# Kernel tuning notes

Measured on AMD Instinct MI355X. Metric: run time of the kernel, lower is better.

Reference implementation:

```python
import jax, jax.numpy as jnp
import numpy as np

K = 2        # kernel_size
DIL = 1      # dilation
H = 768      # h_size = nhid + nout
NOUT = 256
NLAYER = 10  # weight-tied iterations of f_theta


def conv1d(x, w, b, dilation=1):
    # x: (B, Cin, L), w: (Cout, Cin, K) -> (B, Cout, L-(K-1)*dilation)
    y = jax.lax.conv_general_dilated(
        x, w, window_strides=(1,), padding='VALID',
        rhs_dilation=(dilation,), dimension_numbers=('NCH', 'OIH', 'NCH'))
    return y + b[None, :, None]


def setup_inputs() -> dict:
    key = jax.random.key(0)
    ks = jax.random.split(key, 5)
    B, NINP, L = 4, 512, 1024
    bound = 0.01  # init_weights() uses N(0, 0.01)
    return {
        'X': jax.random.normal(ks[0], (B, NINP, L), dtype=jnp.float32),
        'z0': jnp.zeros((B, 2 * H, 1), dtype=jnp.float32),
        'inject_w': bound * jax.random.normal(ks[1], (4 * H, NINP, K), dtype=jnp.float32),
        'inject_b': bound * jax.random.normal(ks[2], (4 * H,), dtype=jnp.float32),
        'conv_w': bound * jax.random.normal(ks[3], (4 * H, H, K), dtype=jnp.float32),
        'conv_b': bound * jax.random.normal(ks[4], (4 * H,), dtype=jnp.float32),
    }


def reference(X, z0, inject_w, inject_b, conv_w, conv_b):
    B, _, L = X.shape
    pad_in = K - 1            # inject conv causal padding
    pad_h = (K - 1) * DIL     # hidden conv causal padding

    # us = inject_conv(pad(X)) : (B, 4H, L), computed once
    Xp = jnp.pad(X, ((0, 0), (0, 0), (pad_in, 0)))
    us = conv1d(Xp, inject_w, inject_b, dilation=1)

    z0h, z0c = z0[:, :H], z0[:, H:]  # (B, H, 1) each
    hid_pad = jnp.broadcast_to(z0h, (B, H, pad_h))  # repeat history into padding

    def step(z1s, _):
        z1h, z1c = z1s[:, :H], z1s[:, H:]
        # shifted cell state: cat([z0c, z1c])[:, :, :-1]
        z0c_s = jnp.concatenate([z0c, z1c[:, :, :-1]], axis=2)
        # weight-tied causal dilated conv on hidden part, history in padding
        xh = jnp.concatenate([hid_pad, z1h], axis=2)
        out = us + conv1d(xh, conv_w, conv_b, dilation=DIL)  # (B, 4H, L)
        it, ot, gt, ft = jnp.split(out, 4, axis=1)
        ct = jax.nn.sigmoid(ft) * z0c_s + jax.nn.sigmoid(it) * jnp.tanh(gt)
        ht = jax.nn.sigmoid(ot) * jnp.tanh(ct)
        return jnp.concatenate([ht, ct], axis=1), None

    z1s0 = jnp.zeros((B, 2 * H, L), dtype=X.dtype)
    z1s, _ = jax.lax.scan(step, z1s0, None, length=NLAYER)

    out = jnp.transpose(z1s[:, H - NOUT:H], (0, 2, 1))  # (B, L, nout)
    z0_out = z1s[:, :, -1:]                              # history repackaging
    return out, z0_out
```

## Files before the change

### kernel.cpp

```cpp
#include <hip/hip_runtime.h>
#include <hip/hip_bf16.h>
#include <stdint.h>


#define B_    4
#define L_    1024
#define LP1   1025
#define H_    768
#define NG_   3072
#define NINP_ 512
#define NOUT_ 256

typedef __bf16 bf16x8 __attribute__((ext_vector_type(8)));
typedef float f32x4 __attribute__((ext_vector_type(4)));
typedef _Float16 f16x4 __attribute__((ext_vector_type(4)));
using bf16_t = __hip_bfloat16;

__device__ __forceinline__ float sigf(float x){ return 1.f/(1.f + __expf(-x)); }
__device__ __forceinline__ float tanhf_(float x){
  float e = __expf(-2.f*fabsf(x));
  float r = (1.f - e)/(1.f + e);
  return x >= 0.f ? r : -r;
}

__device__ __forceinline__ void gl_lds16(const void* g, void* l){
  __builtin_amdgcn_global_load_lds(
    (const __attribute__((address_space(1))) uint32_t*)g,
    (__attribute__((address_space(3))) uint32_t*)l, 16, 0, 0);
}

__global__ void init_k(const float* __restrict__ z0, bf16_t* __restrict__ Xt,
                       bf16_t* __restrict__ Hb0, bf16_t* __restrict__ Hb1,
                       _Float16* __restrict__ Cb0, _Float16* __restrict__ Cb1){
  int tid = blockIdx.x*256 + threadIdx.x;
  if (tid < B_*NINP_){
    int b = tid >> 9, i = tid & 511;
    Xt[(size_t)b*LP1*NINP_ + i] = __float2bfloat16(0.f);
  }
  if (tid < B_*H_){
    int b = tid / H_, j = tid % H_;
    size_t idx = (size_t)b*LP1*H_ + j;
    bf16_t hz = __float2bfloat16(z0[b*2*H_ + j]);
    _Float16 cz = (_Float16)z0[b*2*H_ + H_ + j];
    Hb0[idx] = hz; Hb1[idx] = hz; Cb0[idx] = cz; Cb1[idx] = cz;
  }
}

__global__ void prep_w(const float* __restrict__ iw, const float* __restrict__ ib,
                       const float* __restrict__ cw, const float* __restrict__ cb,
                       bf16_t* __restrict__ Wit, bf16_t* __restrict__ Wct,
                       float* __restrict__ bias4){
  int op = blockIdx.x;
  int gate = (op >> 4) & 3;
  int j = ((op >> 6) << 4) | (op & 15);
  int o = gate*H_ + j;
  const float2* s2 = (const float2*)(iw + (size_t)o*NINP_*2);
  bf16_t* d = Wit + (size_t)op*(2*NINP_);
  for (int i = threadIdx.x; i < NINP_; i += 256){
    float2 v = s2[i];
    d[i]         = __float2bfloat16(v.x);
    d[NINP_ + i] = __float2bfloat16(v.y);
  }
  const float2* c2 = (const float2*)(cw + (size_t)o*H_*2);
  bf16_t* dc = Wct + (size_t)op*(2*H_);
  for (int i = threadIdx.x; i < H_; i += 256){
    float2 v = c2[i];
    dc[i]      = __float2bfloat16(v.x);
    dc[H_ + i] = __float2bfloat16(v.y);
  }
  if (threadIdx.x == 0) bias4[j*4 + gate] = ib[o] + cb[o];
}

__global__ void transpose_x(const float* __restrict__ X, bf16_t* __restrict__ Xt){
  __shared__ float tile[64][65];
  int b = blockIdx.z;
  int t0 = blockIdx.x*64, i0 = blockIdx.y*64;
  int c = threadIdx.x & 63;
  for (int r = threadIdx.x >> 6; r < 64; r += 4)
    tile[r][c] = X[((size_t)b*NINP_ + i0 + r)*L_ + t0 + c];
  __syncthreads();
  for (int r = threadIdx.x >> 6; r < 64; r += 4)
    Xt[((size_t)b*LP1 + t0 + r + 1)*NINP_ + i0 + c] = __float2bfloat16(tile[c][r]);
}

template<int KTOT, int AROW, int MODE>
__launch_bounds__(256, 3)
__global__ void gemm_fused(const bf16_t* __restrict__ A, const bf16_t* __restrict__ Bt,
                           const float* __restrict__ bias4, f16x4* __restrict__ us4,
                           const _Float16* __restrict__ Cprev, _Float16* __restrict__ Cnew,
                           bf16_t* __restrict__ Hnew, int bn_base){
  __shared__ bf16_t As[128*32];
  __shared__ bf16_t Bs[128*32];
  const int tid = threadIdx.x;
  const int l = tid & 63;
  const int w = tid >> 6;
  const int wm = w >> 1, wn = w & 1;

  const int nwg = gridDim.x * gridDim.y;
  int flat = blockIdx.y * gridDim.x + blockIdx.x;
  flat = (flat & 7) * (nwg >> 3) + (flat >> 3);
  const int bm0 = (flat & 31) * 128;
  const int bn0 = bn_base + (flat >> 5) * 128;

  f32x4 acc[4][4];
#pragma unroll
  for (int i = 0; i < 4; ++i)
#pragma unroll
    for (int jj = 0; jj < 4; ++jj)
      acc[i][jj] = (f32x4){0.f,0.f,0.f,0.f};

  const int sr = l >> 2;
  const int sb = (l & 3) << 4;
  const char* ag[2]; const char* bg[2];
  char* al[2]; char* bl[2];
#pragma unroll
  for (int n = 0; n < 2; ++n){
    const int r = w*16 + n*64 + sr;
    const int m = bm0 + r;
    const int b = m >> 10, t = m & 1023;
    ag[n] = (const char*)A + ((size_t)(b*LP1 + t)*AROW)*2 + sb;
    bg[n] = (const char*)Bt + ((size_t)(bn0 + r)*KTOT)*2 + sb;
    al[n] = (char*)As + (w + n*4)*1024;
    bl[n] = (char*)Bs + (w + n*4)*1024;
  }

  const int kg = (l >> 4) << 4;
  const int lr = l & 15;

  for (int kt = 0; kt < KTOT/32; ++kt){
    const int ko = kt << 6;
    gl_lds16(ag[0] + ko, al[0]);
    gl_lds16(ag[1] + ko, al[1]);
    gl_lds16(bg[0] + ko, bl[0]);
    gl_lds16(bg[1] + ko, bl[1]);
    __syncthreads();
    bf16x8 af[4], bfv[4];
#pragma unroll
    for (int f = 0; f < 4; ++f){
      af[f]  = *reinterpret_cast<const bf16x8*>((const char*)As + (wm*64 + f*16 + lr)*64 + kg);
      bfv[f] = *reinterpret_cast<const bf16x8*>((const char*)Bs + (wn*64 + f*16 + lr)*64 + kg);
    }
#pragma unroll
    for (int fm = 0; fm < 4; ++fm)
#pragma unroll
      for (int fn = 0; fn < 4; ++fn)
        acc[fm][fn] = __builtin_amdgcn_mfma_f32_16x16x32_bf16(af[fm], bfv[fn], acc[fm][fn], 0, 0, 0);
    __syncthreads();
  }

  const int jblk = (bn0 + wn*64) >> 6;
  const int j = jblk*16 + lr;
  const int rq = (l >> 4) << 2;

  if (MODE == 0){
    const float4 bz = ((const float4*)bias4)[j];
#pragma unroll
    for (int fm = 0; fm < 4; ++fm){
      const int mbase = bm0 + wm*64 + fm*16 + rq;
#pragma unroll
      for (int r = 0; r < 4; ++r){
        const int m = mbase + r;
        f16x4 v = { (_Float16)(acc[fm][0][r] + bz.x), (_Float16)(acc[fm][1][r] + bz.y),
                    (_Float16)(acc[fm][2][r] + bz.z), (_Float16)(acc[fm][3][r] + bz.w) };
        us4[(size_t)m*H_ + j] = v;
      }
    }
  } else {
#pragma unroll
    for (int fm = 0; fm < 4; ++fm){
      const int mbase = bm0 + wm*64 + fm*16 + rq;
      f16x4 uv[4]; _Float16 cp16[4]; size_t hcb[4];
#pragma unroll
      for (int r = 0; r < 4; ++r){
        const int m = mbase + r;
        const int b = m >> 10, t = m & 1023;
        uv[r] = us4[(size_t)m*H_ + j];
        hcb[r] = (size_t)(b*LP1 + t)*H_ + j;
        cp16[r] = Cprev[hcb[r]];
      }
#pragma unroll
      for (int r = 0; r < 4; ++r){
        const float ig = acc[fm][0][r] + (float)uv[r][0];
        const float og = acc[fm][1][r] + (float)uv[r][1];
        const float gg = acc[fm][2][r] + (float)uv[r][2];
        const float fg = acc[fm][3][r] + (float)uv[r][3];
        const float c  = sigf(fg)*(float)cp16[r] + sigf(ig)*tanhf_(gg);
        const float h  = sigf(og)*tanhf_(c);
        Cnew[hcb[r] + H_] = (_Float16)c;
        Hnew[hcb[r] + H_] = __float2bfloat16(h);
      }
    }
  }
}

__global__ void iter0_k(const f16x4* __restrict__ us4, bf16_t* __restrict__ Hn,
                        _Float16* __restrict__ Cn){
  const int m = blockIdx.y;
  const int j = blockIdx.x*256 + threadIdx.x;
  const int b = m >> 10, t = m & 1023;
  f16x4 u = us4[(size_t)m*H_ + j];
  const float ig = (float)u[0], og = (float)u[1], gg = (float)u[2], fg = (float)u[3];
  float cp = (t == 0) ? (float)Cn[(size_t)b*LP1*H_ + j] : 0.f;
  const float c = sigf(fg)*cp + sigf(ig)*tanhf_(gg);
  const float h = sigf(og)*tanhf_(c);
  const size_t idx = (size_t)(b*LP1 + t + 1)*H_ + j;
  Cn[idx] = (_Float16)c;
  Hn[idx] = __float2bfloat16(h);
}

__global__ void tail_k(const bf16_t* __restrict__ H8, const _Float16* __restrict__ C8,
                       const f16x4* __restrict__ us4, const bf16_t* __restrict__ Wct,
                       float* __restrict__ out){
  const int b = blockIdx.y;
  const int op = blockIdx.x*256 + threadIdx.x;
  const int gate = (op >> 4) & 3, lr = op & 15;
  const int j = ((op >> 6) << 4) | lr;
  const bf16_t* a  = H8 + (size_t)(b*LP1 + 1023)*H_;
  const bf16_t* wr = Wct + (size_t)op*1536;
  float s = 0.f;
#pragma unroll 4
  for (int k2 = 0; k2 < 1536; k2 += 8){
    bf16x8 av = *reinterpret_cast<const bf16x8*>(a + k2);
    bf16x8 wv = *reinterpret_cast<const bf16x8*>(wr + k2);
#pragma unroll
    for (int u = 0; u < 8; ++u) s += (float)av[u]*(float)wv[u];
  }
  s += (float)us4[(size_t)(b*1024 + 1023)*H_ + j][gate];
  const float si = __shfl(s, lr);
  const float so = __shfl(s, lr + 16);
  const float sg = __shfl(s, lr + 32);
  const float sf = __shfl(s, lr + 48);
  if (gate == 0){
    const float cp = (float)C8[(size_t)(b*LP1 + 1023)*H_ + j];
    const float c = sigf(sf)*cp + sigf(si)*tanhf_(sg);
    const float h = sigf(so)*tanhf_(c);
    out[B_*L_*NOUT_ + b*2*H_ + j]      = h;
    out[B_*L_*NOUT_ + b*2*H_ + H_ + j] = c;
  }
}

__global__ void finalize_k(const bf16_t* __restrict__ Hf, float* __restrict__ out){
  const int tid = blockIdx.x*256 + threadIdx.x;
  const int n = tid & 255, t = (tid >> 8) & 1023, b = tid >> 18;
  out[tid] = __bfloat162float(Hf[((size_t)b*LP1 + t + 1)*H_ + (H_ - NOUT_) + n]);
}

extern "C" void kernel_launch(void* const* d_in, const int* in_sizes, int n_in,
                              void* d_out, int out_size, void* d_ws, size_t ws_size,
                              hipStream_t stream){
  const float* X   = (const float*)d_in[0];
  const float* z0  = (const float*)d_in[1];
  const float* iw  = (const float*)d_in[2];
  const float* ib  = (const float*)d_in[3];
  const float* cw  = (const float*)d_in[4];
  const float* cbv = (const float*)d_in[5];
  float* out = (float*)d_out;

  char* ws = (char*)d_ws;
  f16x4*    us4  = (f16x4*)   (ws + 0);
  bf16_t*   Xt   = (bf16_t*)  (ws + 25165824);
  bf16_t*   Wit  = (bf16_t*)  (ws + 29364224);
  bf16_t*   Wct  = (bf16_t*)  (ws + 35655680);
  float*    bias4= (float*)   (ws + 45092864);
  bf16_t*   Hb0  = (bf16_t*)  (ws + 45105152);
  bf16_t*   Hb1  = (bf16_t*)  (ws + 51402752);
  _Float16* Cb0  = (_Float16*)(ws + 57700352);
  _Float16* Cb1  = (_Float16*)(ws + 63997952);

  init_k<<<12, 256, 0, stream>>>(z0, Xt, Hb0, Hb1, Cb0, Cb1);
  prep_w<<<NG_, 256, 0, stream>>>(iw, ib, cw, cbv, Wit, Wct, bias4);
  transpose_x<<<dim3(L_/64, NINP_/64, B_), 256, 0, stream>>>(X, Xt);

  gemm_fused<1024, NINP_, 0><<<dim3(32, 24), 256, 0, stream>>>(
      Xt, Wit, bias4, us4, nullptr, nullptr, nullptr, 0);

  iter0_k<<<dim3(3, 4096), 256, 0, stream>>>(us4, Hb0, Cb0);

  bf16_t* Hp = Hb0; _Float16* Cp = Cb0;
  bf16_t* Hn = Hb1; _Float16* Cn = Cb1;
  for (int it = 1; it <= 8; ++it){
    gemm_fused<1536, H_, 1><<<dim3(32, 24), 256, 0, stream>>>(
        Hp, Wct, nullptr, us4, Cp, Cn, Hn, 0);
    bf16_t* th = Hp; Hp = Hn; Hn = th;
    _Float16* tc = Cp; Cp = Cn; Cn = tc;
  }

  tail_k<<<dim3(12, B_), 256, 0, stream>>>(Hp, Cp, us4, Wct, out);

  gemm_fused<1536, H_, 1><<<dim3(32, 8), 256, 0, stream>>>(
      Hp, Wct, nullptr, us4, Cp, Cn, Hn, 2048);

  finalize_k<<<4096, 256, 0, stream>>>(Hn, out);
}
```

Baseline: 628.2 us.

## Use 256x256 tiles with 4-stage LDS pipeline and drop partial last iteration

Replaces the 128x128 GEMM with a 512-thread 256x256-tile kernel that keeps four LDS stages in flight, uses an XOR swizzle to avoid bank conflicts and raises MFMA issue priority. The last iteration now runs the full GEMM instead of a tail kernel plus a partial-column GEMM, and finalize writes the history outputs. The aim is more reuse per loaded byte and load latency hidden behind math. In exchange it needs 128KB of dynamic LDS, gives 192 workgroups (low occupancy) and does redundant work in the final iteration.

```diff
diff --git a/kernel.cpp b/kernel.cpp
--- a/kernel.cpp
+++ b/kernel.cpp
@@ -84,79 +84,106 @@
 }
 
 template<int KTOT, int AROW, int MODE>
-__launch_bounds__(256, 3)
-__global__ void gemm_fused(const bf16_t* __restrict__ A, const bf16_t* __restrict__ Bt,
-                           const float* __restrict__ bias4, f16x4* __restrict__ us4,
-                           const _Float16* __restrict__ Cprev, _Float16* __restrict__ Cnew,
-                           bf16_t* __restrict__ Hnew, int bn_base){
-  __shared__ bf16_t As[128*32];
-  __shared__ bf16_t Bs[128*32];
+__launch_bounds__(512, 2)
+__global__ void gemm8(const bf16_t* __restrict__ A, const bf16_t* __restrict__ Bt,
+                      const float* __restrict__ bias4, f16x4* __restrict__ us4,
+                      const _Float16* __restrict__ Cprev, _Float16* __restrict__ Cnew,
+                      bf16_t* __restrict__ Hnew){
+  extern __shared__ char smem[];
+  char* AsB = smem;
+  char* BsB = smem + 65536;
+
   const int tid = threadIdx.x;
-  const int l = tid & 63;
-  const int w = tid >> 6;
-  const int wm = w >> 1, wn = w & 1;
+  const int l  = tid & 63;
+  const int w  = tid >> 6;
+  const int wm = w >> 2, wn = w & 3;
 
   const int nwg = gridDim.x * gridDim.y;
   int flat = blockIdx.y * gridDim.x + blockIdx.x;
   flat = (flat & 7) * (nwg >> 3) + (flat >> 3);
-  const int bm0 = (flat & 31) * 128;
-  const int bn0 = bn_base + (flat >> 5) * 128;
-
-  f32x4 acc[4][4];
-#pragma unroll
-  for (int i = 0; i < 4; ++i)
+  const int bm0 = (flat & 15) * 256;
+  const int bn0 = (flat >> 4) * 256;
+
+  f32x4 acc[8][4];
+#pragma unroll
+  for (int i = 0; i < 8; ++i)
 #pragma unroll
     for (int jj = 0; jj < 4; ++jj)
       acc[i][jj] = (f32x4){0.f,0.f,0.f,0.f};
 
-  const int sr = l >> 2;
-  const int sb = (l & 3) << 4;
+  const int kgs = (l & 3) ^ ((l >> 4) & 3);
   const char* ag[2]; const char* bg[2];
-  char* al[2]; char* bl[2];
+  int al[2];
 #pragma unroll
   for (int n = 0; n < 2; ++n){
-    const int r = w*16 + n*64 + sr;
+    const int r = (n*8 + w)*16 + (l >> 2);
     const int m = bm0 + r;
     const int b = m >> 10, t = m & 1023;
-    ag[n] = (const char*)A + ((size_t)(b*LP1 + t)*AROW)*2 + sb;
-    bg[n] = (const char*)Bt + ((size_t)(bn0 + r)*KTOT)*2 + sb;
-    al[n] = (char*)As + (w + n*4)*1024;
-    bl[n] = (char*)Bs + (w + n*4)*1024;
-  }
-
-  const int kg = (l >> 4) << 4;
-  const int lr = l & 15;
-
-  for (int kt = 0; kt < KTOT/32; ++kt){
-    const int ko = kt << 6;
-    gl_lds16(ag[0] + ko, al[0]);
-    gl_lds16(ag[1] + ko, al[1]);
-    gl_lds16(bg[0] + ko, bl[0]);
-    gl_lds16(bg[1] + ko, bl[1]);
-    __syncthreads();
-    bf16x8 af[4], bfv[4];
-#pragma unroll
-    for (int f = 0; f < 4; ++f){
-      af[f]  = *reinterpret_cast<const bf16x8*>((const char*)As + (wm*64 + f*16 + lr)*64 + kg);
-      bfv[f] = *reinterpret_cast<const bf16x8*>((const char*)Bs + (wn*64 + f*16 + lr)*64 + kg);
-    }
-#pragma unroll
-    for (int fm = 0; fm < 4; ++fm)
-#pragma unroll
-      for (int fn = 0; fn < 4; ++fn)
-        acc[fm][fn] = __builtin_amdgcn_mfma_f32_16x16x32_bf16(af[fm], bfv[fn], acc[fm][fn], 0, 0, 0);
-    __syncthreads();
-  }
-
-  const int jblk = (bn0 + wn*64) >> 6;
+    ag[n] = (const char*)A + (size_t)(b*LP1 + t)*(AROW*2) + kgs*16;
+    bg[n] = (const char*)Bt + (size_t)(bn0 + r)*(KTOT*2) + kgs*16;
+    al[n] = (n*8 + w)*1024;
+  }
+
+  const int lr = l & 15, kg = l >> 4;
+  const int xq = (kg ^ ((lr >> 2) & 3)) << 4;
+  const int aoff = (wm*128 + lr)*64 + xq;
+  const int boff = (wn*64  + lr)*64 + xq;
+
+#define STAGE(T) { \
+    char* ad = AsB + (((T) & 3) << 14); \
+    char* bd = BsB + (((T) & 3) << 14); \
+    const int ko = (T) << 6; \
+    gl_lds16(ag[0] + ko, ad + al[0]); \
+    gl_lds16(ag[1] + ko, ad + al[1]); \
+    gl_lds16(bg[0] + ko, bd + al[0]); \
+    gl_lds16(bg[1] + ko, bd + al[1]); }
+
+#define COMPUTE(T) { \
+    const char* ab = AsB + (((T) & 3) << 14); \
+    const char* bb = BsB + (((T) & 3) << 14); \
+    bf16x8 af[8], bv[4]; \
+    _Pragma("unroll") for (int f = 0; f < 8; ++f) \
+      af[f] = *(const bf16x8*)(ab + aoff + f*1024); \
+    _Pragma("unroll") for (int f = 0; f < 4; ++f) \
+      bv[f] = *(const bf16x8*)(bb + boff + f*1024); \
+    __builtin_amdgcn_s_setprio(1); \
+    _Pragma("unroll") for (int fm = 0; fm < 8; ++fm) \
+      _Pragma("unroll") for (int fn = 0; fn < 4; ++fn) \
+        acc[fm][fn] = __builtin_amdgcn_mfma_f32_16x16x32_bf16(af[fm], bv[fn], acc[fm][fn], 0, 0, 0); \
+    __builtin_amdgcn_s_setprio(0); }
+
+  constexpr int NT = KTOT / 32;
+
+  STAGE(0) STAGE(1) STAGE(2)
+  asm volatile("s_waitcnt vmcnt(8)" ::: "memory");
+  __builtin_amdgcn_s_barrier();
+
+  for (int t = 0; t < NT - 3; ++t){
+    STAGE(t+3)
+    COMPUTE(t)
+    asm volatile("s_waitcnt vmcnt(8)" ::: "memory");
+    __builtin_amdgcn_s_barrier();
+  }
+  COMPUTE(NT-3)
+  asm volatile("s_waitcnt vmcnt(4)" ::: "memory");
+  __builtin_amdgcn_s_barrier();
+  COMPUTE(NT-2)
+  asm volatile("s_waitcnt vmcnt(0)" ::: "memory");
+  __builtin_amdgcn_s_barrier();
+  COMPUTE(NT-1)
+
+#undef STAGE
+#undef COMPUTE
+
+  const int jblk = (bn0 >> 6) + wn;
   const int j = jblk*16 + lr;
-  const int rq = (l >> 4) << 2;
+  const int rq = kg << 2;
 
   if (MODE == 0){
     const float4 bz = ((const float4*)bias4)[j];
 #pragma unroll
-    for (int fm = 0; fm < 4; ++fm){
-      const int mbase = bm0 + wm*64 + fm*16 + rq;
+    for (int fm = 0; fm < 8; ++fm){
+      const int mbase = bm0 + wm*128 + fm*16 + rq;
 #pragma unroll
       for (int r = 0; r < 4; ++r){
         const int m = mbase + r;
@@ -167,8 +194,8 @@
     }
   } else {
 #pragma unroll
-    for (int fm = 0; fm < 4; ++fm){
-      const int mbase = bm0 + wm*64 + fm*16 + rq;
+    for (int fm = 0; fm < 8; ++fm){
+      const int mbase = bm0 + wm*128 + fm*16 + rq;
       f16x4 uv[4]; _Float16 cp16[4]; size_t hcb[4];
 #pragma unroll
       for (int r = 0; r < 4; ++r){
@@ -208,41 +235,18 @@
   Hn[idx] = __float2bfloat16(h);
 }
 
-__global__ void tail_k(const bf16_t* __restrict__ H8, const _Float16* __restrict__ C8,
-                       const f16x4* __restrict__ us4, const bf16_t* __restrict__ Wct,
-                       float* __restrict__ out){
-  const int b = blockIdx.y;
-  const int op = blockIdx.x*256 + threadIdx.x;
-  const int gate = (op >> 4) & 3, lr = op & 15;
-  const int j = ((op >> 6) << 4) | lr;
-  const bf16_t* a  = H8 + (size_t)(b*LP1 + 1023)*H_;
-  const bf16_t* wr = Wct + (size_t)op*1536;
-  float s = 0.f;
-#pragma unroll 4
-  for (int k2 = 0; k2 < 1536; k2 += 8){
-    bf16x8 av = *reinterpret_cast<const bf16x8*>(a + k2);
-    bf16x8 wv = *reinterpret_cast<const bf16x8*>(wr + k2);
-#pragma unroll
-    for (int u = 0; u < 8; ++u) s += (float)av[u]*(float)wv[u];
-  }
-  s += (float)us4[(size_t)(b*1024 + 1023)*H_ + j][gate];
-  const float si = __shfl(s, lr);
-  const float so = __shfl(s, lr + 16);
-  const float sg = __shfl(s, lr + 32);
-  const float sf = __shfl(s, lr + 48);
-  if (gate == 0){
-    const float cp = (float)C8[(size_t)(b*LP1 + 1023)*H_ + j];
-    const float c = sigf(sf)*cp + sigf(si)*tanhf_(sg);
-    const float h = sigf(so)*tanhf_(c);
-    out[B_*L_*NOUT_ + b*2*H_ + j]      = h;
-    out[B_*L_*NOUT_ + b*2*H_ + H_ + j] = c;
-  }
-}
-
-__global__ void finalize_k(const bf16_t* __restrict__ Hf, float* __restrict__ out){
+__global__ void finalize_k(const bf16_t* __restrict__ Hf, const _Float16* __restrict__ Cf,
+                           float* __restrict__ out){
   const int tid = blockIdx.x*256 + threadIdx.x;
-  const int n = tid & 255, t = (tid >> 8) & 1023, b = tid >> 18;
-  out[tid] = __bfloat162float(Hf[((size_t)b*LP1 + t + 1)*H_ + (H_ - NOUT_) + n]);
+  if (tid < B_*L_*NOUT_){
+    const int n = tid & 255, t = (tid >> 8) & 1023, b = tid >> 18;
+    out[tid] = __bfloat162float(Hf[((size_t)b*LP1 + t + 1)*H_ + (H_ - NOUT_) + n]);
+  } else if (tid < B_*L_*NOUT_ + B_*2*H_){
+    const int r = tid - B_*L_*NOUT_;
+    const int b = r / (2*H_), ch = r % (2*H_);
+    const size_t row = ((size_t)b*LP1 + L_)*H_;
+    out[tid] = (ch < H_) ? __bfloat162float(Hf[row + ch]) : (float)Cf[row + (ch - H_)];
+  }
 }
 
 extern "C" void kernel_launch(void* const* d_in, const int* in_sizes, int n_in,
@@ -267,28 +271,28 @@
   _Float16* Cb0  = (_Float16*)(ws + 57700352);
   _Float16* Cb1  = (_Float16*)(ws + 63997952);
 
+  hipFuncSetAttribute((const void*)gemm8<1024, NINP_, 0>,
+                      hipFuncAttributeMaxDynamicSharedMemorySize, 131072);
+  hipFuncSetAttribute((const void*)gemm8<1536, H_, 1>,
+                      hipFuncAttributeMaxDynamicSharedMemorySize, 131072);
+
   init_k<<<12, 256, 0, stream>>>(z0, Xt, Hb0, Hb1, Cb0, Cb1);
   prep_w<<<NG_, 256, 0, stream>>>(iw, ib, cw, cbv, Wit, Wct, bias4);
   transpose_x<<<dim3(L_/64, NINP_/64, B_), 256, 0, stream>>>(X, Xt);
 
-  gemm_fused<1024, NINP_, 0><<<dim3(32, 24), 256, 0, stream>>>(
-      Xt, Wit, bias4, us4, nullptr, nullptr, nullptr, 0);
+  gemm8<1024, NINP_, 0><<<dim3(16, 12), 512, 131072, stream>>>(
+      Xt, Wit, bias4, us4, nullptr, nullptr, nullptr);
 
   iter0_k<<<dim3(3, 4096), 256, 0, stream>>>(us4, Hb0, Cb0);
 
   bf16_t* Hp = Hb0; _Float16* Cp = Cb0;
   bf16_t* Hn = Hb1; _Float16* Cn = Cb1;
-  for (int it = 1; it <= 8; ++it){
-    gemm_fused<1536, H_, 1><<<dim3(32, 24), 256, 0, stream>>>(
-        Hp, Wct, nullptr, us4, Cp, Cn, Hn, 0);
+  for (int it = 1; it <= 9; ++it){
+    gemm8<1536, H_, 1><<<dim3(16, 12), 512, 131072, stream>>>(
+        Hp, Wct, nullptr, us4, Cp, Cn, Hn);
     bf16_t* th = Hp; Hp = Hn; Hn = th;
     _Float16* tc = Cp; Cp = Cn; Cn = tc;
   }
 
-  tail_k<<<dim3(12, B_), 256, 0, stream>>>(Hp, Cp, us4, Wct, out);
-
-  gemm_fused<1536, H_, 1><<<dim3(32, 8), 256, 0, stream>>>(
-      Hp, Wct, nullptr, us4, Cp, Cn, Hn, 2048);
-
-  finalize_k<<<4096, 256, 0, stream>>>(Hn, out);
-}
+  finalize_k<<<4120, 256, 0, stream>>>(Hp, Cp, out);
+}
```

New measurement: 645.4 us. 2.7% more time.

## Triple-buffer LDS in fused GEMM with async prefetch two tiles ahead

Applied to the files above, without the earlier changes.

Replaces the single-buffered load/sync/compute loop in the fused GEMM with a three-slot LDS ring. Each K tile is prefetched two steps ahead via global-to-LDS loads, gated by vmcnt waits and a single barrier per step. It also reorders the staged layout so each lane reads one contiguous 16-byte fragment, and raises wave priority around the MFMA block. LDS per block grows to 48KB, which may limit the three-blocks-per-CU occupancy target, and correctness now depends on the hand-counted vmcnt values.

```diff
diff --git a/kernel.cpp b/kernel.cpp
--- a/kernel.cpp
+++ b/kernel.cpp
@@ -85,16 +85,18 @@
 
 template<int KTOT, int AROW, int MODE>
 __launch_bounds__(256, 3)
-__global__ void gemm_fused(const bf16_t* __restrict__ A, const bf16_t* __restrict__ Bt,
-                           const float* __restrict__ bias4, f16x4* __restrict__ us4,
-                           const _Float16* __restrict__ Cprev, _Float16* __restrict__ Cnew,
-                           bf16_t* __restrict__ Hnew, int bn_base){
-  __shared__ bf16_t As[128*32];
-  __shared__ bf16_t Bs[128*32];
+__global__ void gemmF(const bf16_t* __restrict__ A, const bf16_t* __restrict__ Bt,
+                      const float* __restrict__ bias4, f16x4* __restrict__ us4,
+                      const _Float16* __restrict__ Cprev, _Float16* __restrict__ Cnew,
+                      bf16_t* __restrict__ Hnew, int bn_base){
+  __shared__ __align__(1024) char smem[49152];
+
   const int tid = threadIdx.x;
-  const int l = tid & 63;
-  const int w = tid >> 6;
+  const int l  = tid & 63;
+  const int w  = tid >> 6;
   const int wm = w >> 1, wn = w & 1;
+  const int lr = l & 15;
+  const int lk = l >> 4;
 
   const int nwg = gridDim.x * gridDim.y;
   int flat = blockIdx.y * gridDim.x + blockIdx.x;
@@ -109,48 +111,62 @@
     for (int jj = 0; jj < 4; ++jj)
       acc[i][jj] = (f32x4){0.f,0.f,0.f,0.f};
 
-  const int sr = l >> 2;
-  const int sb = (l & 3) << 4;
   const char* ag[2]; const char* bg[2];
-  char* al[2]; char* bl[2];
 #pragma unroll
   for (int n = 0; n < 2; ++n){
-    const int r = w*16 + n*64 + sr;
-    const int m = bm0 + r;
+    const int mf = w*2 + n;
+    const int m = bm0 + mf*16 + lr;
     const int b = m >> 10, t = m & 1023;
-    ag[n] = (const char*)A + ((size_t)(b*LP1 + t)*AROW)*2 + sb;
-    bg[n] = (const char*)Bt + ((size_t)(bn0 + r)*KTOT)*2 + sb;
-    al[n] = (char*)As + (w + n*4)*1024;
-    bl[n] = (char*)Bs + (w + n*4)*1024;
-  }
-
-  const int kg = (l >> 4) << 4;
-  const int lr = l & 15;
-
-  for (int kt = 0; kt < KTOT/32; ++kt){
-    const int ko = kt << 6;
-    gl_lds16(ag[0] + ko, al[0]);
-    gl_lds16(ag[1] + ko, al[1]);
-    gl_lds16(bg[0] + ko, bl[0]);
-    gl_lds16(bg[1] + ko, bl[1]);
-    __syncthreads();
-    bf16x8 af[4], bfv[4];
-#pragma unroll
-    for (int f = 0; f < 4; ++f){
-      af[f]  = *reinterpret_cast<const bf16x8*>((const char*)As + (wm*64 + f*16 + lr)*64 + kg);
-      bfv[f] = *reinterpret_cast<const bf16x8*>((const char*)Bs + (wn*64 + f*16 + lr)*64 + kg);
+    ag[n] = (const char*)A + (size_t)(b*LP1 + t)*(AROW*2) + lk*16;
+    const int nc = bn0 + mf*16 + lr;
+    bg[n] = (const char*)Bt + (size_t)nc*(KTOT*2) + lk*16;
+  }
+  const int a0off = (w*2    )*1024;
+  const int a1off = (w*2 + 1)*1024;
+
+#define STAGE_AT(S, KO) { \
+    char* base_ = smem + (S)*16384; \
+    gl_lds16(ag[0] + (KO), base_ + a0off); \
+    gl_lds16(ag[1] + (KO), base_ + a1off); \
+    gl_lds16(bg[0] + (KO), base_ + 8192 + a0off); \
+    gl_lds16(bg[1] + (KO), base_ + 8192 + a1off); }
+
+#define COMPUTE_AT(S) { \
+    const char* sp_ = smem + (S)*16384 + l*16; \
+    bf16x8 af[4], bv[4]; \
+    _Pragma("unroll") for (int f = 0; f < 4; ++f) \
+      af[f] = *(const bf16x8*)(sp_ + (wm*4 + f)*1024); \
+    _Pragma("unroll") for (int f = 0; f < 4; ++f) \
+      bv[f] = *(const bf16x8*)(sp_ + 8192 + (wn*4 + f)*1024); \
+    __builtin_amdgcn_s_setprio(1); \
+    _Pragma("unroll") for (int fm = 0; fm < 4; ++fm) \
+      _Pragma("unroll") for (int fn = 0; fn < 4; ++fn) \
+        acc[fm][fn] = __builtin_amdgcn_mfma_f32_16x16x32_bf16(af[fm], bv[fn], acc[fm][fn], 0, 0, 0); \
+    __builtin_amdgcn_s_setprio(0); }
+
+  constexpr int NT = KTOT / 32;
+
+  STAGE_AT(0, 0)
+  STAGE_AT(1, 64)
+  int slot = 0;
+  for (int t = 0; t < NT; ++t){
+    if (t < NT - 1) { asm volatile("s_waitcnt vmcnt(4)" ::: "memory"); }
+    else            { asm volatile("s_waitcnt vmcnt(0)" ::: "memory"); }
+    __builtin_amdgcn_s_barrier();
+    if (t + 2 < NT){
+      const int s2 = (slot >= 1) ? slot - 1 : 2;
+      STAGE_AT(s2, (t + 2) << 6)
     }
-#pragma unroll
-    for (int fm = 0; fm < 4; ++fm)
-#pragma unroll
-      for (int fn = 0; fn < 4; ++fn)
-        acc[fm][fn] = __builtin_amdgcn_mfma_f32_16x16x32_bf16(af[fm], bfv[fn], acc[fm][fn], 0, 0, 0);
-    __syncthreads();
-  }
-
-  const int jblk = (bn0 + wn*64) >> 6;
+    COMPUTE_AT(slot)
+    slot = (slot < 2) ? slot + 1 : 0;
+  }
+
+#undef STAGE_AT
+#undef COMPUTE_AT
+
+  const int jblk = (bn0 >> 6) + wn;
   const int j = jblk*16 + lr;
-  const int rq = (l >> 4) << 2;
+  const int rq = lk << 2;
 
   if (MODE == 0){
     const float4 bz = ((const float4*)bias4)[j];
@@ -271,7 +287,7 @@
   prep_w<<<NG_, 256, 0, stream>>>(iw, ib, cw, cbv, Wit, Wct, bias4);
   transpose_x<<<dim3(L_/64, NINP_/64, B_), 256, 0, stream>>>(X, Xt);
 
-  gemm_fused<1024, NINP_, 0><<<dim3(32, 24), 256, 0, stream>>>(
+  gemmF<1024, NINP_, 0><<<dim3(32, 24), 256, 0, stream>>>(
       Xt, Wit, bias4, us4, nullptr, nullptr, nullptr, 0);
 
   iter0_k<<<dim3(3, 4096), 256, 0, stream>>>(us4, Hb0, Cb0);
@@ -279,7 +295,7 @@
   bf16_t* Hp = Hb0; _Float16* Cp = Cb0;
   bf16_t* Hn = Hb1; _Float16* Cn = Cb1;
   for (int it = 1; it <= 8; ++it){
-    gemm_fused<1536, H_, 1><<<dim3(32, 24), 256, 0, stream>>>(
+    gemmF<1536, H_, 1><<<dim3(32, 24), 256, 0, stream>>>(
         Hp, Wct, nullptr, us4, Cp, Cn, Hn, 0);
     bf16_t* th = Hp; Hp = Hn; Hn = th;
     _Float16* tc = Cp; Cp = Cn; Cn = tc;
@@ -287,7 +303,7 @@
 
   tail_k<<<dim3(12, B_), 256, 0, stream>>>(Hp, Cp, us4, Wct, out);
 
-  gemm_fused<1536, H_, 1><<<dim3(32, 8), 256, 0, stream>>>(
+  gemmF<1536, H_, 1><<<dim3(32, 8), 256, 0, stream>>>(
       Hp, Wct, nullptr, us4, Cp, Cn, Hn, 2048);
 
   finalize_k<<<4096, 256, 0, stream>>>(Hn, out);
```

Result: slower. 808.9 us (+28.8%).
